# Performance work log

Measured on AMD Instinct MI355X. Metric: run time of the kernel, lower is better.

Reference implementation:

```python
import jax, jax.numpy as jnp
import numpy as np

N, E, H, D_IN, D_OUT, DEPTH, G = 100000, 1600000, 128, 128, 10, 3, 256


def setup_inputs() -> dict:
    key = jax.random.key(0)
    ks = jax.random.split(key, 16)
    s = lambda k, shape: jax.random.normal(k, shape, dtype=jnp.float32) * 0.05
    inp = {
        "x": jax.random.normal(ks[0], (N, D_IN), dtype=jnp.float32),
        "edge_index": jax.random.randint(ks[1], (2, E), 0, N, dtype=jnp.int32),
        "control_edge_index": jax.random.randint(ks[2], (2, 1024), 0, N, dtype=jnp.int32),
        "batch": jnp.sort(jax.random.randint(ks[3], (N,), 0, G, dtype=jnp.int32)),
        # encoder MLP: input_dim -> hidden -> hidden
        "enc_w1": s(ks[4], (D_IN, H)), "enc_b1": jnp.zeros((H,), jnp.float32),
        "enc_w2": s(ks[5], (H, H)),    "enc_b2": jnp.zeros((H,), jnp.float32),
        # conv_depth GCN layers, hidden -> hidden
        "conv_w": s(ks[6], (DEPTH, H, H)), "conv_b": jnp.zeros((DEPTH, H), jnp.float32),
        # decoder MLP: hidden -> hidden -> output_dim
        "dec_w1": s(ks[7], (H, H)),     "dec_b1": jnp.zeros((H,), jnp.float32),
        "dec_w2": s(ks[8], (H, D_OUT)), "dec_b2": jnp.zeros((D_OUT,), jnp.float32),
    }
    return inp


def _gcn_forward(x, enc_w1, enc_b1, enc_w2, enc_b2, conv_w, conv_b,
                 dec_w1, dec_b1, dec_w2, dec_b2, edge_index, batch):
    # encoder MLP (Linear-ReLU-Dropout(eval)-Linear)
    h = jax.nn.relu(x @ enc_w1 + enc_b1) @ enc_w2 + enc_b2

    # GCN normalization with self-loops: D^{-1/2} (A + I) D^{-1/2}
    loops = jnp.arange(N, dtype=edge_index.dtype)
    src = jnp.concatenate([edge_index[0], loops])  # [E + N]
    dst = jnp.concatenate([edge_index[1], loops])
    deg = jax.ops.segment_sum(jnp.ones_like(src, dtype=h.dtype), dst, num_segments=N)
    inv_sqrt = jax.lax.rsqrt(deg)  # deg >= 1 thanks to self-loops
    coef = (inv_sqrt[src] * inv_sqrt[dst])[:, None]  # [E+N, 1]

    for l in range(DEPTH):
        hw = h @ conv_w[l] + conv_b[l]                      # [N, H]
        h = jax.ops.segment_sum(hw[src] * coef, dst, num_segments=N)
        if l < DEPTH - 1:  # linear=False -> nonlinearity between convs
            h = jax.nn.relu(h)

    # global_add_pool over graph ids
    pooled = jax.ops.segment_sum(h, batch, num_segments=G)   # [G, H]

    # decoder MLP
    return jax.nn.relu(pooled @ dec_w1 + dec_b1) @ dec_w2 + dec_b2  # [G, D_OUT]


def reference(x, edge_index, control_edge_index, batch, enc_w1, enc_b1, enc_w2,
              enc_b2, conv_w, conv_b, dec_w1, dec_b1, dec_w2, dec_b2):
    # control_edge_index corresponds to the (disabled) control mechanism; unused
    return _gcn_forward(x, enc_w1, enc_b1, enc_w2, enc_b2, conv_w, conv_b,
                        dec_w1, dec_b1, dec_w2, dec_b2, edge_index, batch)
```

## Files before the change

### kernel.cpp

```cpp
#include <hip/hip_runtime.h>
#include <hip/hip_bf16.h>
#include <cstdint>
#include <cstddef>

#define NN 100000
#define NE 1600000
#define HH 128
#define NG 256

#define NB 196
#define BSH 9
#define BMSK 511
#define CHUNK 16384
#define NBLK 98

typedef __bf16 bf16x8 __attribute__((ext_vector_type(8)));
typedef float floatx4 __attribute__((ext_vector_type(4)));

__device__ __forceinline__ uint32_t f2b(float f) {
  union { float f; uint32_t u; } v; v.f = f;
  uint32_t u = v.u;
  return (u + 0x7FFFu + ((u >> 16) & 1u)) >> 16;
}
__device__ __forceinline__ float b2f(uint32_t h) {
  union { uint32_t u; float f; } v; v.u = h << 16;
  return v.f;
}
__device__ __forceinline__ void addrow(float* a, uint4 v) {
  a[0] += b2f(v.x & 0xFFFFu); a[1] += b2f(v.x >> 16);
  a[2] += b2f(v.y & 0xFFFFu); a[3] += b2f(v.y >> 16);
  a[4] += b2f(v.z & 0xFFFFu); a[5] += b2f(v.z >> 16);
  a[6] += b2f(v.w & 0xFFFFu); a[7] += b2f(v.w >> 16);
}


__global__ __launch_bounds__(256) void k_cntA(const int* __restrict__ src,
                                              int* __restrict__ blkcnt) {
  __shared__ int h[NB];
  int t = threadIdx.x;
  if (t < NB) h[t] = 0;
  __syncthreads();
  int base = blockIdx.x * CHUNK, end = min(base + CHUNK, NE);
  for (int i = base + t; i < end; i += 256) atomicAdd(&h[src[i] >> BSH], 1);
  __syncthreads();
  if (t < NB) blkcnt[blockIdx.x * NB + t] = h[t];
}

__global__ __launch_bounds__(256) void k_cntB(const uint2* __restrict__ pairs,
                                              int* __restrict__ blkcnt) {
  __shared__ int h[NB];
  int t = threadIdx.x;
  if (t < NB) h[t] = 0;
  __syncthreads();
  int base = blockIdx.x * CHUNK, end = min(base + CHUNK, NE);
  for (int i = base + t; i < end; i += 256) atomicAdd(&h[pairs[i].y >> BSH], 1);
  __syncthreads();
  if (t < NB) blkcnt[blockIdx.x * NB + t] = h[t];
}

__global__ __launch_bounds__(64) void k_colscan(const int* __restrict__ blkcnt,
                                                int* __restrict__ poff,
                                                int* __restrict__ colsum) {
  int b = blockIdx.x, t = threadIdx.x;
  int carry = 0;
  for (int base = 0; base < NBLK; base += 64) {
    int r = base + t;
    int x = (r < NBLK) ? blkcnt[r * NB + b] : 0;
    int v = x;
    for (int d = 1; d < 64; d <<= 1) { int u = __shfl_up(v, d); if (t >= d) v += u; }
    if (r < NBLK) poff[r * NB + b] = carry + v - x;
    carry += __shfl(v, 63);
  }
  if (t == 0) colsum[b] = carry;
}

__global__ void k_gscan(const int* __restrict__ colsum, int* __restrict__ gbase,
                        int* __restrict__ off, int set_off) {
  __shared__ int s[256];
  int t = threadIdx.x;
  int x = (t < NB) ? colsum[t] : 0;
  s[t] = x; __syncthreads();
  for (int d = 1; d < 256; d <<= 1) {
    int v = (t >= d) ? s[t - d] : 0;
    __syncthreads();
    s[t] += v;
    __syncthreads();
  }
  if (t < NB) gbase[t] = s[t] - x;
  if (t == 0) { gbase[NB] = NE; if (set_off) off[NN] = NE; }
}

__global__ __launch_bounds__(256) void k_placeA(const int* __restrict__ src,
                                                const int* __restrict__ dst,
                                                const int* __restrict__ poff,
                                                const int* __restrict__ gbase,
                                                uint2* __restrict__ pairs) {
  __shared__ int cur[NB];
  int t = threadIdx.x;
  if (t < NB) cur[t] = poff[blockIdx.x * NB + t] + gbase[t];
  __syncthreads();
  int base = blockIdx.x * CHUNK, end = min(base + CHUNK, NE);
  for (int i = base + t; i < end; i += 256) {
    int s = src[i], d = dst[i];
    int p = atomicAdd(&cur[s >> BSH], 1);
    pairs[p] = make_uint2((unsigned)s, (unsigned)d);
  }
}

__global__ __launch_bounds__(256) void k_placeB(const uint2* __restrict__ pairs,
                                                const int* __restrict__ poff,
                                                const int* __restrict__ gbase,
                                                uint32_t* __restrict__ outb) {
  __shared__ int cur[NB];
  int t = threadIdx.x;
  if (t < NB) cur[t] = poff[blockIdx.x * NB + t] + gbase[t];
  __syncthreads();
  int base = blockIdx.x * CHUNK, end = min(base + CHUNK, NE);
  for (int i = base + t; i < end; i += 256) {
    uint2 v = pairs[i];
    int p = atomicAdd(&cur[v.y >> BSH], 1);
    outb[p] = v.x | ((v.y & (unsigned)BMSK) << 17);
  }
}

__global__ __launch_bounds__(256) void k_bucket_sort(
    const uint32_t* __restrict__ pairbuf, const int* __restrict__ gbase,
    int* __restrict__ off, float* __restrict__ inv, int* __restrict__ csrs)
{
  __shared__ int cnt[512];
  __shared__ int loff[512];
  __shared__ int psum[256];
  int b = blockIdx.x;
  int tid = threadIdx.x;
  cnt[tid] = 0; cnt[tid + 256] = 0;
  __syncthreads();
  int s0 = gbase[b], s1 = gbase[b + 1];
  for (int i = s0 + tid; i < s1; i += 256)
    atomicAdd(&cnt[pairbuf[i] >> 17], 1);
  __syncthreads();
  int a0 = cnt[2 * tid], a1 = cnt[2 * tid + 1];
  int s = a0 + a1;
  psum[tid] = s;
  __syncthreads();
  for (int d = 1; d < 256; d <<= 1) {
    int v = (tid >= d) ? psum[tid - d] : 0;
    __syncthreads();
    psum[tid] += v;
    __syncthreads();
  }
  int excl = psum[tid] - s;
  loff[2 * tid] = excl;
  loff[2 * tid + 1] = excl + a0;
  __syncthreads();
#pragma unroll
  for (int k = 0; k < 2; ++k) {
    int i = tid + k * 256;
    int node = b * 512 + i;
    if (node < NN) {
      off[node] = s0 + loff[i];
      inv[node] = rsqrtf((float)cnt[i] + 1.0f);
    }
  }
  __syncthreads();
  cnt[tid] = loff[tid]; cnt[tid + 256] = loff[tid + 256];
  __syncthreads();
  for (int i = s0 + tid; i < s1; i += 256) {
    uint32_t v = pairbuf[i];
    int p = atomicAdd(&cnt[v >> 17], 1);
    csrs[s0 + p] = (int)(v & 0x1FFFFu);
  }
}

__global__ __launch_bounds__(256) void k_nodeprep(const int* __restrict__ off,
                                                  const int* __restrict__ batch,
                                                  int* __restrict__ dhist,
                                                  int* __restrict__ gstart) {
  __shared__ int h[64];
  int t = threadIdx.x;
  if (t < 64) h[t] = 0;
  __syncthreads();
  int i = blockIdx.x * 256 + t;
  if (i < NN) {
    int d = off[i + 1] - off[i]; if (d > 63) d = 63;
    atomicAdd(&h[d], 1);
    int b = batch[i];
    if (i == 0) {
      for (int g = 0; g <= b; ++g) gstart[g] = 0;
    } else {
      int a = batch[i - 1];
      for (int g = a + 1; g <= b; ++g) gstart[g] = i;
    }
    if (i == NN - 1) {
      for (int g = b + 1; g <= NG; ++g) gstart[g] = NN;
    }
  }
  __syncthreads();
  if (t < 64 && h[t]) atomicAdd(&dhist[t], h[t]);
}

__global__ void k_dscan(const int* __restrict__ dhist, int* __restrict__ dcur) {
  int t = threadIdx.x;
  int x = dhist[63 - t];
  int v = x;
  for (int d = 1; d < 64; d <<= 1) { int u = __shfl_up(v, d); if (t >= d) v += u; }
  dcur[63 - t] = v - x;
}

__global__ __launch_bounds__(256) void k_dplace(const int* __restrict__ off,
                                                int* __restrict__ dcur,
                                                int* __restrict__ order) {
  __shared__ int h[64], base[64];
  int t = threadIdx.x;
  if (t < 64) h[t] = 0;
  __syncthreads();
  int i = blockIdx.x * 256 + t;
  int d = 0, ld = 0;
  if (i < NN) { d = off[i + 1] - off[i]; if (d > 63) d = 63; ld = atomicAdd(&h[d], 1); }
  __syncthreads();
  if (t < 64) base[t] = h[t] ? atomicAdd(&dcur[t], h[t]) : 0;
  __syncthreads();
  if (i < NN) order[base[d] + ld] = i;
}

__global__ __launch_bounds__(256) void k_gemm(
    const uint16_t* __restrict__ A16, const float* __restrict__ A32,
    const float* __restrict__ W, const float* __restrict__ bias,
    const float* __restrict__ scale,
    uint16_t* __restrict__ Out, int M, int do_relu)
{
  __shared__ uint16_t Wt[128][136];
  const int tid = threadIdx.x;

  for (int it = 0; it < 16; ++it) {
    int idx = tid + it * 256;
    int n = idx & 127;
    int k0 = (idx >> 7) * 4;
    uint2 wv;
    wv.x = f2b(W[(k0 + 0) * 128 + n]) | (f2b(W[(k0 + 1) * 128 + n]) << 16);
    wv.y = f2b(W[(k0 + 2) * 128 + n]) | (f2b(W[(k0 + 3) * 128 + n]) << 16);
    *(uint2*)&Wt[n][k0] = wv;
  }
  __syncthreads();

  const int lane = tid & 63;
  const int wave = tid >> 6;
  const int lrow = lane & 15;
  const int lk = (lane >> 4) * 8;
  const int row0 = blockIdx.x * 128 + wave * 32;

  floatx4 acc[2][8];
#pragma unroll
  for (int t = 0; t < 2; ++t)
#pragma unroll
    for (int n = 0; n < 8; ++n)
      acc[t][n] = (floatx4){0.f, 0.f, 0.f, 0.f};

#pragma unroll
  for (int ks = 0; ks < 4; ++ks) {
    bf16x8 a[2];
#pragma unroll
    for (int t = 0; t < 2; ++t) {
      int r = row0 + t * 16 + lrow;
      uint4 tmp = {0u, 0u, 0u, 0u};
      if (r < M) {
        if (A32) {
          float4 f0 = *(const float4*)(A32 + (size_t)r * HH + ks * 32 + lk);
          float4 f1 = *(const float4*)(A32 + (size_t)r * HH + ks * 32 + lk + 4);
          tmp.x = f2b(f0.x) | (f2b(f0.y) << 16);
          tmp.y = f2b(f0.z) | (f2b(f0.w) << 16);
          tmp.z = f2b(f1.x) | (f2b(f1.y) << 16);
          tmp.w = f2b(f1.z) | (f2b(f1.w) << 16);
        } else {
          tmp = *(const uint4*)(A16 + (size_t)r * HH + ks * 32 + lk);
        }
      }
      a[t] = __builtin_bit_cast(bf16x8, tmp);
    }
#pragma unroll
    for (int n = 0; n < 8; ++n) {
      bf16x8 b = __builtin_bit_cast(bf16x8, *(const uint4*)&Wt[n * 16 + lrow][ks * 32 + lk]);
      acc[0][n] = __builtin_amdgcn_mfma_f32_16x16x32_bf16(a[0], b, acc[0][n], 0, 0, 0);
      acc[1][n] = __builtin_amdgcn_mfma_f32_16x16x32_bf16(a[1], b, acc[1][n], 0, 0, 0);
    }
  }

  float bc[8];
#pragma unroll
  for (int n = 0; n < 8; ++n) bc[n] = bias[n * 16 + lrow];

  const int rbase = (lane >> 4) * 4;
#pragma unroll
  for (int t = 0; t < 2; ++t) {
#pragma unroll
    for (int r = 0; r < 4; ++r) {
      int row = row0 + t * 16 + rbase + r;
      if (row < M) {
        float sc = scale ? scale[row] : 1.0f;
#pragma unroll
        for (int n = 0; n < 8; ++n) {
          float v = acc[t][n][r] + bc[n];
          if (do_relu) v = fmaxf(v, 0.f);
          v *= sc;
          Out[(size_t)row * HH + n * 16 + lrow] = (uint16_t)f2b(v);
        }
      }
    }
  }
}

__global__ __launch_bounds__(256) void k_agg(
    const uint16_t* __restrict__ hw2, const int* __restrict__ off,
    const int* __restrict__ csrs, const float* __restrict__ inv,
    const int* __restrict__ order,
    uint16_t* __restrict__ hout, int do_relu)
{
  int slot = blockIdx.x * 16 + (threadIdx.x >> 4);
  if (slot >= NN) return;
  int node = order[slot];
  int c = (threadIdx.x & 15) * 8;

  uint4 sv = *(const uint4*)(hw2 + (size_t)node * HH + c);
  float a[8] = {0.f, 0.f, 0.f, 0.f, 0.f, 0.f, 0.f, 0.f};
  addrow(a, sv);

  int e0 = off[node], e1 = off[node + 1];
  int e = e0;
  for (; e + 8 <= e1; e += 8) {
    int s[8];
#pragma unroll
    for (int k = 0; k < 8; ++k) s[k] = csrs[e + k];
    uint4 v[8];
#pragma unroll
    for (int k = 0; k < 8; ++k) v[k] = *(const uint4*)(hw2 + (size_t)s[k] * HH + c);
#pragma unroll
    for (int k = 0; k < 8; ++k) addrow(a, v[k]);
  }
  for (; e < e1; ++e) {
    int s = csrs[e];
    uint4 v = *(const uint4*)(hw2 + (size_t)s * HH + c);
    addrow(a, v);
  }
  float invd = inv[node];
#pragma unroll
  for (int j = 0; j < 8; ++j) {
    a[j] *= invd;
    if (do_relu) a[j] = fmaxf(a[j], 0.f);
  }
  uint4 o;
  o.x = f2b(a[0]) | (f2b(a[1]) << 16);
  o.y = f2b(a[2]) | (f2b(a[3]) << 16);
  o.z = f2b(a[4]) | (f2b(a[5]) << 16);
  o.w = f2b(a[6]) | (f2b(a[7]) << 16);
  *(uint4*)(hout + (size_t)node * HH + c) = o;
}

__global__ __launch_bounds__(256) void k_pool(const uint16_t* __restrict__ h,
                                              const int* __restrict__ gstart,
                                              float* __restrict__ pooled) {
  __shared__ float red[16][132];
  int g = blockIdx.x;
  int tid = threadIdx.x;
  int slot = tid >> 4;
  int c = (tid & 15) * 8;

  int r0 = gstart[g], r1 = gstart[g + 1];
  float a[8] = {0.f, 0.f, 0.f, 0.f, 0.f, 0.f, 0.f, 0.f};
  for (int r = r0 + slot; r < r1; r += 16) {
    uint4 v = *(const uint4*)(h + (size_t)r * HH + c);
    a[0] += b2f(v.x & 0xFFFFu); a[1] += b2f(v.x >> 16);
    a[2] += b2f(v.y & 0xFFFFu); a[3] += b2f(v.y >> 16);
    a[4] += b2f(v.z & 0xFFFFu); a[5] += b2f(v.z >> 16);
    a[6] += b2f(v.w & 0xFFFFu); a[7] += b2f(v.w >> 16);
  }
  *(float4*)&red[slot][c]     = make_float4(a[0], a[1], a[2], a[3]);
  *(float4*)&red[slot][c + 4] = make_float4(a[4], a[5], a[6], a[7]);
  __syncthreads();
  if (tid < 128) {
    float s = 0.f;
#pragma unroll
    for (int k = 0; k < 16; ++k) s += red[k][tid];
    pooled[g * HH + tid] = s;
  }
}

__global__ void k_dec(const float* __restrict__ pooled,
                      const float* __restrict__ w1, const float* __restrict__ b1,
                      const float* __restrict__ w2, const float* __restrict__ b2,
                      float* __restrict__ out) {
  __shared__ float p[128], t[128];
  int g = blockIdx.x, j = threadIdx.x;
  p[j] = pooled[g * HH + j];
  __syncthreads();
  float a = b1[j];
  for (int k = 0; k < 128; ++k) a += p[k] * w1[k * 128 + j];
  t[j] = fmaxf(a, 0.f);
  __syncthreads();
  if (j < 10) {
    float o = b2[j];
    for (int k = 0; k < 128; ++k) o += t[k] * w2[k * 10 + j];
    out[g * 10 + j] = o;
  }
}

extern "C" void kernel_launch(void* const* d_in, const int* in_sizes, int n_in,
                              void* d_out, int out_size, void* d_ws, size_t ws_size,
                              hipStream_t stream) {
  const float* x       = (const float*)d_in[0];
  const int*   eidx    = (const int*)d_in[1];
  const int*   src     = eidx;
  const int*   dst     = eidx + NE;
  const int*   batch   = (const int*)d_in[3];
  const float* enc_w1  = (const float*)d_in[4];
  const float* enc_b1  = (const float*)d_in[5];
  const float* enc_w2  = (const float*)d_in[6];
  const float* enc_b2  = (const float*)d_in[7];
  const float* conv_w  = (const float*)d_in[8];
  const float* conv_b  = (const float*)d_in[9];
  const float* dec_w1  = (const float*)d_in[10];
  const float* dec_b1  = (const float*)d_in[11];
  const float* dec_w2  = (const float*)d_in[12];
  const float* dec_b2  = (const float*)d_in[13];
  float* out = (float*)d_out;

  char* ws = (char*)d_ws;
  size_t o = 0;
  auto alloc = [&](size_t bytes) -> char* {
    char* p = ws + o;
    o += (bytes + 255) & ~(size_t)255;
    return p;
  };
  int*      off     = (int*)alloc((size_t)(NN + 1) * 4);
  int*      csrs    = (int*)alloc((size_t)NE * 4);
  float*    inv     = (float*)alloc((size_t)NN * 4);
  float*    pooled  = (float*)alloc((size_t)NG * HH * 4);
  int*      blkcntA = (int*)alloc((size_t)NBLK * NB * 4);
  int*      poffA   = (int*)alloc((size_t)NBLK * NB * 4);
  int*      blkcntB = (int*)alloc((size_t)NBLK * NB * 4);
  int*      poffB   = (int*)alloc((size_t)NBLK * NB * 4);
  int*      colsumA = (int*)alloc((size_t)NB * 4);
  int*      colsumB = (int*)alloc((size_t)NB * 4);
  int*      gbaseA  = (int*)alloc((size_t)(NB + 1) * 4);
  int*      gbaseB  = (int*)alloc((size_t)(NB + 1) * 4);
  int*      dhist   = (int*)alloc(64 * 4);
  int*      dcur    = (int*)alloc(64 * 4);
  int*      order   = (int*)alloc((size_t)NN * 4);
  int*      gstart  = (int*)alloc((size_t)(NG + 1) * 4);
  uint16_t* buf0    = (uint16_t*)alloc((size_t)NN * HH * 2);
  uint16_t* buf1    = (uint16_t*)alloc((size_t)NN * HH * 2);
  uint2*    pairsA  = (uint2*)buf1;
  uint32_t* pairB   = (uint32_t*)((char*)buf1 + (size_t)NE * 8);

  hipMemsetAsync(dhist, 0, 64 * 4, stream);

  k_cntA<<<dim3(NBLK), dim3(256), 0, stream>>>(src, blkcntA);
  k_colscan<<<dim3(NB), dim3(64), 0, stream>>>(blkcntA, poffA, colsumA);
  k_gscan<<<dim3(1), dim3(256), 0, stream>>>(colsumA, gbaseA, off, 0);
  k_placeA<<<dim3(NBLK), dim3(256), 0, stream>>>(src, dst, poffA, gbaseA, pairsA);
  k_cntB<<<dim3(NBLK), dim3(256), 0, stream>>>(pairsA, blkcntB);
  k_colscan<<<dim3(NB), dim3(64), 0, stream>>>(blkcntB, poffB, colsumB);
  k_gscan<<<dim3(1), dim3(256), 0, stream>>>(colsumB, gbaseB, off, 1);
  k_placeB<<<dim3(NBLK), dim3(256), 0, stream>>>(pairsA, poffB, gbaseB, pairB);
  k_bucket_sort<<<dim3(NB), dim3(256), 0, stream>>>(pairB, gbaseB, off, inv, csrs);

  const int NBK = (NN + 255) / 256;
  k_nodeprep<<<dim3(NBK), dim3(256), 0, stream>>>(off, batch, dhist, gstart);
  k_dscan<<<dim3(1), dim3(64), 0, stream>>>(dhist, dcur);
  k_dplace<<<dim3(NBK), dim3(256), 0, stream>>>(off, dcur, order);

  const int GB = (NN + 127) / 128;
  k_gemm<<<dim3(GB), dim3(256), 0, stream>>>(nullptr, x, enc_w1, enc_b1, nullptr, buf1, NN, 1);
  k_gemm<<<dim3(GB), dim3(256), 0, stream>>>(buf1, nullptr, enc_w2, enc_b2, nullptr, buf0, NN, 0);

  const int AB = (NN + 15) / 16;
  k_gemm<<<dim3(GB), dim3(256), 0, stream>>>(buf0, nullptr, conv_w + 0 * 16384, conv_b + 0,   inv, buf1, NN, 0);
  k_agg <<<dim3(AB), dim3(256), 0, stream>>>(buf1, off, csrs, inv, order, buf0, 1);
  k_gemm<<<dim3(GB), dim3(256), 0, stream>>>(buf0, nullptr, conv_w + 1 * 16384, conv_b + 128, inv, buf1, NN, 0);
  k_agg <<<dim3(AB), dim3(256), 0, stream>>>(buf1, off, csrs, inv, order, buf0, 1);
  k_gemm<<<dim3(GB), dim3(256), 0, stream>>>(buf0, nullptr, conv_w + 2 * 16384, conv_b + 256, inv, buf1, NN, 0);
  k_agg <<<dim3(AB), dim3(256), 0, stream>>>(buf1, off, csrs, inv, order, buf0, 0);

  k_pool<<<dim3(NG), dim3(256), 0, stream>>>(buf0, gstart, pooled);
  k_dec<<<dim3(NG), dim3(128), 0, stream>>>(pooled, dec_w1, dec_b1, dec_w2, dec_b2, out);
}
```

Baseline: 537.9 us.

## Fold last GCN layer and add-pool into edge-weighted pooling before the GEMM

```diff
diff --git a/kernel.cpp b/kernel.cpp
--- a/kernel.cpp
+++ b/kernel.cpp
@@ -13,6 +13,9 @@
 #define BMSK 511
 #define CHUNK 16384
 #define NBLK 98
+
+#define EPB ((NE + 97) / 98)
+#define NPB ((NN + 97) / 98)
 
 typedef __bf16 bf16x8 __attribute__((ext_vector_type(8)));
 typedef float floatx4 __attribute__((ext_vector_type(4)));
@@ -171,29 +174,14 @@
   }
 }
 
-__global__ __launch_bounds__(256) void k_nodeprep(const int* __restrict__ off,
-                                                  const int* __restrict__ batch,
-                                                  int* __restrict__ dhist,
-                                                  int* __restrict__ gstart) {
+__global__ __launch_bounds__(256) void k_deghist(const int* __restrict__ off,
+                                                 int* __restrict__ dhist) {
   __shared__ int h[64];
   int t = threadIdx.x;
   if (t < 64) h[t] = 0;
   __syncthreads();
   int i = blockIdx.x * 256 + t;
-  if (i < NN) {
-    int d = off[i + 1] - off[i]; if (d > 63) d = 63;
-    atomicAdd(&h[d], 1);
-    int b = batch[i];
-    if (i == 0) {
-      for (int g = 0; g <= b; ++g) gstart[g] = 0;
-    } else {
-      int a = batch[i - 1];
-      for (int g = a + 1; g <= b; ++g) gstart[g] = i;
-    }
-    if (i == NN - 1) {
-      for (int g = b + 1; g <= NG; ++g) gstart[g] = NN;
-    }
-  }
+  if (i < NN) { int d = off[i + 1] - off[i]; if (d > 63) d = 63; atomicAdd(&h[d], 1); }
   __syncthreads();
   if (t < 64 && h[t]) atomicAdd(&dhist[t], h[t]);
 }
@@ -220,6 +208,18 @@
   if (t < 64) base[t] = h[t] ? atomicAdd(&dcur[t], h[t]) : 0;
   __syncthreads();
   if (i < NN) order[base[d] + ld] = i;
+}
+
+__global__ __launch_bounds__(256) void k_prep_edges(const uint2* __restrict__ pairs,
+                                                    const float* __restrict__ inv,
+                                                    const int* __restrict__ batch,
+                                                    uint32_t* __restrict__ esg,
+                                                    float* __restrict__ ew) {
+  int i = blockIdx.x * 256 + threadIdx.x;
+  if (i >= NE) return;
+  uint2 p = pairs[i];
+  esg[i] = p.x | ((uint32_t)batch[p.y] << 17);
+  ew[i] = inv[p.x] * inv[p.y];
 }
 
 __global__ __launch_bounds__(256) void k_gemm(
@@ -325,15 +325,13 @@
 
   int e0 = off[node], e1 = off[node + 1];
   int e = e0;
-  for (; e + 8 <= e1; e += 8) {
-    int s[8];
-#pragma unroll
-    for (int k = 0; k < 8; ++k) s[k] = csrs[e + k];
-    uint4 v[8];
-#pragma unroll
-    for (int k = 0; k < 8; ++k) v[k] = *(const uint4*)(hw2 + (size_t)s[k] * HH + c);
-#pragma unroll
-    for (int k = 0; k < 8; ++k) addrow(a, v[k]);
+  for (; e + 4 <= e1; e += 4) {
+    int s0 = csrs[e + 0], s1 = csrs[e + 1], s2 = csrs[e + 2], s3 = csrs[e + 3];
+    uint4 v0 = *(const uint4*)(hw2 + (size_t)s0 * HH + c);
+    uint4 v1 = *(const uint4*)(hw2 + (size_t)s1 * HH + c);
+    uint4 v2 = *(const uint4*)(hw2 + (size_t)s2 * HH + c);
+    uint4 v3 = *(const uint4*)(hw2 + (size_t)s3 * HH + c);
+    addrow(a, v0); addrow(a, v1); addrow(a, v2); addrow(a, v3);
   }
   for (; e < e1; ++e) {
     int s = csrs[e];
@@ -354,44 +352,88 @@
   *(uint4*)(hout + (size_t)node * HH + c) = o;
 }
 
-__global__ __launch_bounds__(256) void k_pool(const uint16_t* __restrict__ h,
-                                              const int* __restrict__ gstart,
-                                              float* __restrict__ pooled) {
-  __shared__ float red[16][132];
-  int g = blockIdx.x;
+__global__ __launch_bounds__(256) void k_edgepool(
+    const uint16_t* __restrict__ h2, const uint32_t* __restrict__ esg,
+    const float* __restrict__ ew, const float* __restrict__ inv,
+    const int* __restrict__ batch,
+    float* __restrict__ q, float* __restrict__ S)
+{
+  __shared__ float qlds[NG * 32];
+  __shared__ float slds[NG];
   int tid = threadIdx.x;
-  int slot = tid >> 4;
-  int c = (tid & 15) * 8;
-
-  int r0 = gstart[g], r1 = gstart[g + 1];
-  float a[8] = {0.f, 0.f, 0.f, 0.f, 0.f, 0.f, 0.f, 0.f};
-  for (int r = r0 + slot; r < r1; r += 16) {
-    uint4 v = *(const uint4*)(h + (size_t)r * HH + c);
-    a[0] += b2f(v.x & 0xFFFFu); a[1] += b2f(v.x >> 16);
-    a[2] += b2f(v.y & 0xFFFFu); a[3] += b2f(v.y >> 16);
-    a[4] += b2f(v.z & 0xFFFFu); a[5] += b2f(v.z >> 16);
-    a[6] += b2f(v.w & 0xFFFFu); a[7] += b2f(v.w >> 16);
-  }
-  *(float4*)&red[slot][c]     = make_float4(a[0], a[1], a[2], a[3]);
-  *(float4*)&red[slot][c + 4] = make_float4(a[4], a[5], a[6], a[7]);
-  __syncthreads();
-  if (tid < 128) {
-    float s = 0.f;
-#pragma unroll
-    for (int k = 0; k < 16; ++k) s += red[k][tid];
-    pooled[g * HH + tid] = s;
-  }
-}
-
-__global__ void k_dec(const float* __restrict__ pooled,
+  int y = blockIdx.y;
+  for (int k = tid; k < NG * 32; k += 256) qlds[k] = 0.f;
+  if (tid < NG) slds[tid] = 0.f;
+  __syncthreads();
+
+  int grp = tid >> 2;
+  int ln = tid & 3;
+  int cbase = y * 32 + ln * 8;
+  int do_s = (y == 0 && ln == 0);
+
+  int e0 = blockIdx.x * EPB, e1 = min(e0 + EPB, NE);
+  for (int e = e0 + grp; e < e1; e += 64) {
+    uint32_t sg = esg[e];
+    float w = ew[e];
+    int s = sg & 0x1FFFF;
+    int g = sg >> 17;
+    uint4 v = *(const uint4*)(h2 + (size_t)s * HH + cbase);
+    float* qr = &qlds[g * 32 + ln * 8];
+    atomicAdd(&qr[0], w * b2f(v.x & 0xFFFFu));
+    atomicAdd(&qr[1], w * b2f(v.x >> 16));
+    atomicAdd(&qr[2], w * b2f(v.y & 0xFFFFu));
+    atomicAdd(&qr[3], w * b2f(v.y >> 16));
+    atomicAdd(&qr[4], w * b2f(v.z & 0xFFFFu));
+    atomicAdd(&qr[5], w * b2f(v.z >> 16));
+    atomicAdd(&qr[6], w * b2f(v.w & 0xFFFFu));
+    atomicAdd(&qr[7], w * b2f(v.w >> 16));
+    if (do_s) atomicAdd(&slds[g], w);
+  }
+
+  int n0 = blockIdx.x * NPB, n1 = min(n0 + NPB, NN);
+  for (int i = n0 + grp; i < n1; i += 64) {
+    float iv = inv[i];
+    float w = iv * iv;
+    int g = batch[i];
+    uint4 v = *(const uint4*)(h2 + (size_t)i * HH + cbase);
+    float* qr = &qlds[g * 32 + ln * 8];
+    atomicAdd(&qr[0], w * b2f(v.x & 0xFFFFu));
+    atomicAdd(&qr[1], w * b2f(v.x >> 16));
+    atomicAdd(&qr[2], w * b2f(v.y & 0xFFFFu));
+    atomicAdd(&qr[3], w * b2f(v.y >> 16));
+    atomicAdd(&qr[4], w * b2f(v.z & 0xFFFFu));
+    atomicAdd(&qr[5], w * b2f(v.z >> 16));
+    atomicAdd(&qr[6], w * b2f(v.w & 0xFFFFu));
+    atomicAdd(&qr[7], w * b2f(v.w >> 16));
+    if (do_s) atomicAdd(&slds[g], w);
+  }
+  __syncthreads();
+
+  for (int k = tid; k < NG * 32; k += 256) {
+    float v = qlds[k];
+    if (v != 0.f) atomicAdd(&q[(k >> 5) * HH + y * 32 + (k & 31)], v);
+  }
+  if (y == 0 && tid < NG) {
+    float v = slds[tid];
+    if (v != 0.f) atomicAdd(&S[tid], v);
+  }
+}
+
+__global__ void k_dec(const float* __restrict__ q, const float* __restrict__ S,
+                      const float* __restrict__ Wc, const float* __restrict__ bc,
                       const float* __restrict__ w1, const float* __restrict__ b1,
                       const float* __restrict__ w2, const float* __restrict__ b2,
                       float* __restrict__ out) {
-  __shared__ float p[128], t[128];
+  __shared__ float qs[128], p[128], t[128];
   int g = blockIdx.x, j = threadIdx.x;
-  p[j] = pooled[g * HH + j];
-  __syncthreads();
-  float a = b1[j];
+  qs[j] = q[g * HH + j];
+  __syncthreads();
+  float sg = S[g];
+  float a = sg * bc[j];
+  for (int k = 0; k < 128; ++k) a += qs[k] * Wc[k * 128 + j];
+  p[j] = a;
+  __syncthreads();
+  a = b1[j];
   for (int k = 0; k < 128; ++k) a += p[k] * w1[k * 128 + j];
   t[j] = fmaxf(a, 0.f);
   __syncthreads();
@@ -432,7 +474,6 @@
   int*      off     = (int*)alloc((size_t)(NN + 1) * 4);
   int*      csrs    = (int*)alloc((size_t)NE * 4);
   float*    inv     = (float*)alloc((size_t)NN * 4);
-  float*    pooled  = (float*)alloc((size_t)NG * HH * 4);
   int*      blkcntA = (int*)alloc((size_t)NBLK * NB * 4);
   int*      poffA   = (int*)alloc((size_t)NBLK * NB * 4);
   int*      blkcntB = (int*)alloc((size_t)NBLK * NB * 4);
@@ -444,13 +485,18 @@
   int*      dhist   = (int*)alloc(64 * 4);
   int*      dcur    = (int*)alloc(64 * 4);
   int*      order   = (int*)alloc((size_t)NN * 4);
-  int*      gstart  = (int*)alloc((size_t)(NG + 1) * 4);
+  float*    q       = (float*)alloc((size_t)NG * HH * 4);
+  float*    Sg      = (float*)alloc((size_t)NG * 4);
+  uint2*    pairsA  = (uint2*)alloc((size_t)NE * 8);
+  uint32_t* esg     = (uint32_t*)alloc((size_t)NE * 4);
+  float*    ew      = (float*)alloc((size_t)NE * 4);
   uint16_t* buf0    = (uint16_t*)alloc((size_t)NN * HH * 2);
   uint16_t* buf1    = (uint16_t*)alloc((size_t)NN * HH * 2);
-  uint2*    pairsA  = (uint2*)buf1;
-  uint32_t* pairB   = (uint32_t*)((char*)buf1 + (size_t)NE * 8);
+  uint32_t* pairB   = (uint32_t*)buf1;
 
   hipMemsetAsync(dhist, 0, 64 * 4, stream);
+  hipMemsetAsync(q, 0, (size_t)NG * HH * 4, stream);
+  hipMemsetAsync(Sg, 0, (size_t)NG * 4, stream);
 
   k_cntA<<<dim3(NBLK), dim3(256), 0, stream>>>(src, blkcntA);
   k_colscan<<<dim3(NB), dim3(64), 0, stream>>>(blkcntA, poffA, colsumA);
@@ -463,9 +509,11 @@
   k_bucket_sort<<<dim3(NB), dim3(256), 0, stream>>>(pairB, gbaseB, off, inv, csrs);
 
   const int NBK = (NN + 255) / 256;
-  k_nodeprep<<<dim3(NBK), dim3(256), 0, stream>>>(off, batch, dhist, gstart);
+  k_deghist<<<dim3(NBK), dim3(256), 0, stream>>>(off, dhist);
   k_dscan<<<dim3(1), dim3(64), 0, stream>>>(dhist, dcur);
   k_dplace<<<dim3(NBK), dim3(256), 0, stream>>>(off, dcur, order);
+
+  k_prep_edges<<<dim3((NE + 255) / 256), dim3(256), 0, stream>>>(pairsA, inv, batch, esg, ew);
 
   const int GB = (NN + 127) / 128;
   k_gemm<<<dim3(GB), dim3(256), 0, stream>>>(nullptr, x, enc_w1, enc_b1, nullptr, buf1, NN, 1);
@@ -476,9 +524,9 @@
   k_agg <<<dim3(AB), dim3(256), 0, stream>>>(buf1, off, csrs, inv, order, buf0, 1);
   k_gemm<<<dim3(GB), dim3(256), 0, stream>>>(buf0, nullptr, conv_w + 1 * 16384, conv_b + 128, inv, buf1, NN, 0);
   k_agg <<<dim3(AB), dim3(256), 0, stream>>>(buf1, off, csrs, inv, order, buf0, 1);
-  k_gemm<<<dim3(GB), dim3(256), 0, stream>>>(buf0, nullptr, conv_w + 2 * 16384, conv_b + 256, inv, buf1, NN, 0);
-  k_agg <<<dim3(AB), dim3(256), 0, stream>>>(buf1, off, csrs, inv, order, buf0, 0);
-
-  k_pool<<<dim3(NG), dim3(256), 0, stream>>>(buf0, gstart, pooled);
-  k_dec<<<dim3(NG), dim3(128), 0, stream>>>(pooled, dec_w1, dec_b1, dec_w2, dec_b2, out);
-}
+
+  k_edgepool<<<dim3(98, 4), dim3(256), 0, stream>>>(buf0, esg, ew, inv, batch, q, Sg);
+
+  k_dec<<<dim3(NG), dim3(128), 0, stream>>>(q, Sg, conv_w + 2 * 16384, conv_b + 256,
+                                            dec_w1, dec_b1, dec_w2, dec_b2, out);
+}
```

Result: slower. 1.889 ms (+251.2%).
